# Kernel optimization log

Measured on AMD Instinct MI355X. Metric: run time of the kernel, lower is better.

The kernel has to match this reference:

```python
import jax, jax.numpy as jnp
import numpy as np

N_NODES = 100000
N_EDGES = 640000
NODE_DIM = 128
EDGE_DIM = 64
NUM_HEADS = 4
EPS = 1e-6


def setup_inputs() -> dict:
    key = jax.random.key(0)
    ks = jax.random.split(key, 12)
    s_attn = 1.0 / np.sqrt(NODE_DIM + EDGE_DIM)
    s_ev = 1.0 / np.sqrt(EDGE_DIM)
    s_out = 1.0 / np.sqrt(NODE_DIM)
    return {
        "node_features": jax.random.normal(ks[0], (N_NODES, NODE_DIM), jnp.float32),
        "edge_features": jax.random.normal(ks[1], (N_EDGES, EDGE_DIM), jnp.float32),
        "attn_W": jax.random.uniform(ks[2], (NODE_DIM + EDGE_DIM, NUM_HEADS), jnp.float32, -s_attn, s_attn),
        "attn_b": jax.random.uniform(ks[3], (NUM_HEADS,), jnp.float32, -s_attn, s_attn),
        "ev_W": jax.random.uniform(ks[4], (EDGE_DIM, NODE_DIM), jnp.float32, -s_ev, s_ev),
        "ev_b": jax.random.uniform(ks[5], (NODE_DIM,), jnp.float32, -s_ev, s_ev),
        "out1_W": jax.random.uniform(ks[6], (NODE_DIM, NODE_DIM), jnp.float32, -s_out, s_out),
        "out1_b": jax.random.uniform(ks[7], (NODE_DIM,), jnp.float32, -s_out, s_out),
        "out2_W": jax.random.uniform(ks[8], (NODE_DIM, NODE_DIM), jnp.float32, -s_out, s_out),
        "out2_b": jax.random.uniform(ks[9], (NODE_DIM,), jnp.float32, -s_out, s_out),
        "edge_index": jax.random.randint(ks[10], (2, N_EDGES), 0, N_NODES, jnp.int64 if jax.config.jax_enable_x64 else jnp.int32),
    }


def _segment_softmax_aggregate(values, scores_mean, dst, num_nodes):
    # segment max (empty segments -> -inf, then zeroed, matching torch include_self=False path)
    max_scores = jax.ops.segment_max(scores_mean, dst, num_segments=num_nodes)
    max_scores = jnp.where(jnp.isneginf(max_scores), jnp.zeros_like(max_scores), max_scores)
    exp_scores = jnp.exp(scores_mean - max_scores[dst])            # (E,)
    sum_exp = jax.ops.segment_sum(exp_scores, dst, num_segments=num_nodes)
    attn_weights = exp_scores / (sum_exp[dst] + EPS)               # (E,)
    # weighted scatter-add of edge values into destination nodes
    return jax.ops.segment_sum(values * attn_weights[:, None], dst, num_segments=num_nodes)


def reference(node_features, edge_features, attn_W, attn_b, ev_W, ev_b,
              out1_W, out1_b, out2_W, out2_b, edge_index):
    num_nodes = node_features.shape[0]
    dst = edge_index[1]
    h_dst = node_features[dst]                                     # (E, node_dim) gather
    attn_input = jnp.concatenate([h_dst, edge_features], axis=1)   # (E, node_dim+edge_dim)
    attn_scores = attn_input @ attn_W + attn_b                     # (E, H)
    scores_mean = attn_scores.mean(axis=1)                         # (E,)
    edge_values = edge_features @ ev_W + ev_b                      # (E, node_dim)
    messages = _segment_softmax_aggregate(edge_values, scores_mean, dst, num_nodes)
    update = jax.nn.relu(messages @ out1_W + out1_b) @ out2_W + out2_b
    return node_features + update
```

## Files before the change

kernel.cpp:

```cpp
#include <hip/hip_runtime.h>
#include <cstddef>

#define NN 100000
#define NE 640000
#define NB_SCAN 391
#define NTILE 1563

typedef short  short8   __attribute__((ext_vector_type(8)));
typedef float  f32x4    __attribute__((ext_vector_type(4)));
typedef ushort ushort4v __attribute__((ext_vector_type(4)));

__device__ __forceinline__ short f2bf(float f) {
    union { float f; unsigned u; } v; v.f = f;
    unsigned r = (v.u + 0x7fffu + ((v.u >> 16) & 1u)) >> 16;
    return (short)r;
}

__global__ __launch_bounds__(256) void k_init(
    int4* __restrict__ zp, const float* __restrict__ evW,
    const float* __restrict__ evb, const float* __restrict__ W1,
    ushort* __restrict__ EVW1t, float* __restrict__ EVB1)
{
    const int b = blockIdx.x;
    if (b < 196) {
        const int i = b * 256 + threadIdx.x;
        if (i < 50000) zp[i] = make_int4(0, 0, 0, 0);
        return;
    }
    if (threadIdx.x >= 128) return;
    const int j = b - 196;
    const int n = threadIdx.x;
    float acc = 0.f;
    #pragma unroll 8
    for (int c = 0; c < 128; ++c)
        acc = fmaf(evW[j * 128 + c], W1[c * 128 + n], acc);
    EVW1t[n * 64 + j] = (ushort)f2bf(acc);
    if (j == 0) {
        float ab = 0.f;
        #pragma unroll 8
        for (int c = 0; c < 128; ++c)
            ab = fmaf(evb[c], W1[c * 128 + n], ab);
        EVB1[n] = ab;
    }
}

__global__ __launch_bounds__(256) void k_pre(
    const float* __restrict__ W2, const int* __restrict__ dst_idx,
    int* __restrict__ count, ushort* __restrict__ W2t)
{
    const int gid = blockIdx.x * 256 + threadIdx.x;
    if (gid < 16384) {
        const int n = gid >> 7, k = gid & 127;
        W2t[gid] = (ushort)f2bf(W2[k * 128 + n]);
    }
    atomicAdd(&count[dst_idx[gid]], 1);
}

__global__ __launch_bounds__(256) void k_scan_bsum(
    const int* __restrict__ count, int* __restrict__ bsum)
{
    __shared__ int s[256];
    const int t = threadIdx.x, i = blockIdx.x * 256 + t;
    s[t] = (i < NN) ? count[i] : 0;
    __syncthreads();
    for (int off = 128; off; off >>= 1) { if (t < off) s[t] += s[t + off]; __syncthreads(); }
    if (t == 0) bsum[blockIdx.x] = s[0];
}

__global__ __launch_bounds__(256) void k_scan_final(
    const int* __restrict__ count, const int* __restrict__ bsum,
    int* __restrict__ rowptr)
{
    __shared__ int s[256];
    __shared__ int red[4];
    const int t = threadIdx.x, i = blockIdx.x * 256 + t;
    const int v = (i < NN) ? count[i] : 0;
    s[t] = v;

    int part = 0;
    for (int b = t; b < blockIdx.x; b += 256) part += bsum[b];
    #pragma unroll
    for (int off = 32; off; off >>= 1) part += __shfl_xor(part, off);
    if ((t & 63) == 0) red[t >> 6] = part;
    __syncthreads();
    const int boff = red[0] + red[1] + red[2] + red[3];

    for (int off = 1; off < 256; off <<= 1) {
        const int x = (t >= off) ? s[t - off] : 0;
        __syncthreads();
        s[t] += x;
        __syncthreads();
    }
    if (i < NN) rowptr[i] = boff + s[t] - v;
    if (blockIdx.x == NB_SCAN - 1 && t == 255) rowptr[NN] = boff + s[255];
}

__global__ __launch_bounds__(256) void k_permute(
    const int* __restrict__ dst_idx, const int* __restrict__ rowptr,
    int* cursor, int* __restrict__ perm)
{
    const int e = blockIdx.x * 256 + threadIdx.x;
    const int dd = dst_idx[e];
    perm[rowptr[dd] + atomicAdd(&cursor[dd], 1)] = e;
}

__global__ __launch_bounds__(256, 8) void k_agg_gather(
    const float* __restrict__ ef, const float* __restrict__ attn_W,
    const int* __restrict__ perm, const int* __restrict__ rowptr,
    ushort* __restrict__ agg, float* __restrict__ msum)
{
    const int t  = threadIdx.x;
    const int sl = t & 15;
    const int n  = blockIdx.x * 16 + (t >> 4);
    const int beg = rowptr[n], end = rowptr[n + 1];

    float4 wl;
    {
        const float4 r0 = *reinterpret_cast<const float4*>(attn_W + (128 + sl * 4 + 0) * 4);
        const float4 r1 = *reinterpret_cast<const float4*>(attn_W + (128 + sl * 4 + 1) * 4);
        const float4 r2 = *reinterpret_cast<const float4*>(attn_W + (128 + sl * 4 + 2) * 4);
        const float4 r3 = *reinterpret_cast<const float4*>(attn_W + (128 + sl * 4 + 3) * 4);
        wl.x = 0.25f * (r0.x + r0.y + r0.z + r0.w);
        wl.y = 0.25f * (r1.x + r1.y + r1.z + r1.w);
        wl.z = 0.25f * (r2.x + r2.y + r2.z + r2.w);
        wl.w = 0.25f * (r3.x + r3.y + r3.z + r3.w);
    }

    float m  = -3.0e38f;
    float se = 0.f;
    f32x4 acc = {0.f, 0.f, 0.f, 0.f};

    for (int i = beg; i < end; i += 6) {
        int pe[6];
        #pragma unroll
        for (int j = 0; j < 6; ++j)
            pe[j] = perm[(i + j < end) ? (i + j) : beg];
        float4 v[6];
        #pragma unroll
        for (int j = 0; j < 6; ++j)
            v[j] = *reinterpret_cast<const float4*>(ef + (size_t)pe[j] * 64 + sl * 4);
        float sc[6];
        #pragma unroll
        for (int j = 0; j < 6; ++j) {
            float x = v[j].x * wl.x + v[j].y * wl.y + v[j].z * wl.z + v[j].w * wl.w;
            #pragma unroll
            for (int off = 8; off; off >>= 1) x += __shfl_xor(x, off, 16);
            sc[j] = (i + j < end) ? x : -3.0e38f;
        }
        float bm = m;
        #pragma unroll
        for (int j = 0; j < 6; ++j) bm = fmaxf(bm, sc[j]);
        const float r = __expf(m - bm);
        acc[0] *= r; acc[1] *= r; acc[2] *= r; acc[3] *= r; se *= r;
        m = bm;
        #pragma unroll
        for (int j = 0; j < 6; ++j) {
            const float w = __expf(sc[j] - m);
            acc[0] = fmaf(w, v[j].x, acc[0]);
            acc[1] = fmaf(w, v[j].y, acc[1]);
            acc[2] = fmaf(w, v[j].z, acc[2]);
            acc[3] = fmaf(w, v[j].w, acc[3]);
            se += w;
        }
    }

    ushort4v o;
    o[0] = (ushort)f2bf(acc[0]); o[1] = (ushort)f2bf(acc[1]);
    o[2] = (ushort)f2bf(acc[2]); o[3] = (ushort)f2bf(acc[3]);
    *reinterpret_cast<ushort4v*>(agg + (size_t)n * 64 + sl * 4) = o;
    if (sl == 0) msum[n] = se;
}

__global__ __launch_bounds__(256, 2) void k_mega(
    const ushort* __restrict__ agg, const float* __restrict__ msum,
    const ushort* __restrict__ EVW1t, const float* __restrict__ EVB1,
    const float* __restrict__ b1, const ushort* __restrict__ W2t,
    const float* __restrict__ b2, const float* __restrict__ nf,
    float* __restrict__ out)
{
    __shared__ ushort wev[128 * 64];
    __shared__ ushort ww2[128 * 128];
    __shared__ ushort tl[4][16][136];

    const int tid  = threadIdx.x;
    const int wid  = tid >> 6;
    const int lane = tid & 63;
    const int r    = lane & 15;
    const int g    = lane >> 4;

    for (int c = tid; c < 1024; c += 256) {
        const int n = c >> 3, k8 = c & 7;
        *reinterpret_cast<short8*>(&wev[n * 64 + ((k8 ^ (n & 7)) * 8)]) =
            *reinterpret_cast<const short8*>(EVW1t + n * 64 + k8 * 8);
    }
    for (int c = tid; c < 2048; c += 256) {
        const int n = c >> 4, k8 = c & 15;
        *reinterpret_cast<short8*>(&ww2[n * 128 + ((k8 ^ (n & 7)) * 8)]) =
            *reinterpret_cast<const short8*>(W2t + n * 128 + k8 * 8);
    }
    __syncthreads();

    float evb1c[8], b1c[8], b2c[8];
    #pragma unroll
    for (int nt = 0; nt < 8; ++nt) {
        evb1c[nt] = EVB1[nt * 16 + r];
        b1c[nt]   = b1[nt * 16 + r];
        b2c[nt]   = b2[nt * 16 + r];
    }

    for (int bt = blockIdx.x; bt < NTILE; bt += gridDim.x) {
        const int n0 = bt * 64 + wid * 16;
        if (n0 >= NN) continue;

        const short8 aev0 = *reinterpret_cast<const short8*>(agg + (size_t)(n0 + r) * 64 + g * 8);
        const short8 aev1 = *reinterpret_cast<const short8*>(agg + (size_t)(n0 + r) * 64 + 32 + g * 8);
        float cf[4], cb[4];
        #pragma unroll
        for (int i = 0; i < 4; ++i) {
            const float s = msum[n0 + g * 4 + i];
            const float c = 1.f / (s + 1e-6f);
            cf[i] = c; cb[i] = s * c;
        }

        #pragma unroll
        for (int nt = 0; nt < 8; ++nt) {
            const int row = nt * 16 + r;
            const short8 w0 = *reinterpret_cast<const short8*>(
                &wev[row * 64 + (((0 + g) ^ (r & 7)) * 8)]);
            const short8 w1 = *reinterpret_cast<const short8*>(
                &wev[row * 64 + (((4 + g) ^ (r & 7)) * 8)]);
            f32x4 acc = {0.f, 0.f, 0.f, 0.f};
            acc = __builtin_amdgcn_mfma_f32_16x16x32_bf16(aev0, w0, acc, 0, 0, 0);
            acc = __builtin_amdgcn_mfma_f32_16x16x32_bf16(aev1, w1, acc, 0, 0, 0);
            #pragma unroll
            for (int i = 0; i < 4; ++i) {
                const float h = fmaxf(cf[i] * acc[i] + cb[i] * evb1c[nt] + b1c[nt], 0.f);
                tl[wid][g * 4 + i][nt * 16 + r] = (ushort)f2bf(h);
            }
        }
        asm volatile("s_waitcnt lgkmcnt(0)" ::: "memory");

        short8 a2[4];
        #pragma unroll
        for (int t = 0; t < 4; ++t)
            a2[t] = *reinterpret_cast<const short8*>(&tl[wid][r][t * 32 + g * 8]);
        asm volatile("s_waitcnt lgkmcnt(0)" ::: "memory");

        #pragma unroll
        for (int nt = 0; nt < 8; ++nt) {
            f32x4 acc = {0.f, 0.f, 0.f, 0.f};
            #pragma unroll
            for (int t = 0; t < 4; ++t) {
                const short8 w = *reinterpret_cast<const short8*>(
                    &ww2[(nt * 16 + r) * 128 + (((t * 4 + g) ^ (r & 7)) * 8)]);
                acc = __builtin_amdgcn_mfma_f32_16x16x32_bf16(a2[t], w, acc, 0, 0, 0);
            }
            #pragma unroll
            for (int i = 0; i < 4; ++i) {
                const size_t idx = (size_t)(n0 + g * 4 + i) * 128 + nt * 16 + r;
                out[idx] = nf[idx] + acc[i] + b2c[nt];
            }
        }
    }
}

extern "C" void kernel_launch(void* const* d_in, const int* in_sizes, int n_in,
                              void* d_out, int out_size, void* d_ws, size_t ws_size,
                              hipStream_t stream)
{
    const float* nf     = (const float*)d_in[0];
    const float* ef     = (const float*)d_in[1];
    const float* attn_W = (const float*)d_in[2];
    const float* evW    = (const float*)d_in[4];
    const float* evb    = (const float*)d_in[5];
    const float* W1     = (const float*)d_in[6];
    const float* b1     = (const float*)d_in[7];
    const float* W2     = (const float*)d_in[8];
    const float* b2     = (const float*)d_in[9];
    const int*   eidx   = (const int*)d_in[10];
    const int*   dst    = eidx + NE;
    float* out = (float*)d_out;

    char* ws = (char*)d_ws;
    int*    count  = (int*)   (ws + 0);
    int*    cursor = (int*)   (ws + 400000);
    int*    rowptr = (int*)   (ws + 800000);
    float*  msum   = (float*) (ws + 1200128);
    int*    perm   = (int*)   (ws + 1600128);
    ushort* agg    = (ushort*)(ws + 4160128);
    ushort* W2t    = (ushort*)(ws + 16960128);
    ushort* EVW1t  = (ushort*)(ws + 16992896);
    float*  EVB1   = (float*) (ws + 17009280);
    int*    bsum   = (int*)   (ws + 17009792);

    k_init       <<<260,  256, 0, stream>>>((int4*)count, evW, evb, W1, EVW1t, EVB1);
    k_pre        <<<2500, 256, 0, stream>>>(W2, dst, count, W2t);
    k_scan_bsum  <<<NB_SCAN, 256, 0, stream>>>(count, bsum);
    k_scan_final <<<NB_SCAN, 256, 0, stream>>>(count, bsum, rowptr);
    k_permute    <<<2500, 256, 0, stream>>>(dst, rowptr, cursor, perm);
    k_agg_gather <<<6250, 256, 0, stream>>>(ef, attn_W, perm, rowptr, agg, msum);
    k_mega       <<<521,  256, 0, stream>>>(agg, msum, EVW1t, EVB1, b1, W2t, b2, nf, out);
}
```

Baseline: 144.8 us.

## Software-pipeline k_mega tiles with register prefetch of agg, msum and node features

The grid-stride loop in the final MLP kernel becomes three fixed, unrolled tile stages. The next tile's aggregated messages, softmax sums and residual node features are loaded into registers while the current tile's MFMA work runs, and the first tile's loads are issued before the weights are staged into LDS. This is meant to hide global-memory latency, including the residual nf read that previously sat on the store path. It costs many more live registers (two tiles' worth, including 32 floats of nf each) under launch_bounds(256,2), which risks spilling, and it hardcodes three tiles per block to match the grid of 521.

```diff
diff --git a/kernel.cpp b/kernel.cpp
--- a/kernel.cpp
+++ b/kernel.cpp
@@ -5,6 +5,7 @@
 #define NE 640000
 #define NB_SCAN 391
 #define NTILE 1563
+#define MGRID 521
 
 typedef short  short8   __attribute__((ext_vector_type(8)));
 typedef float  f32x4    __attribute__((ext_vector_type(4)));
@@ -171,6 +172,85 @@
     if (sl == 0) msum[n] = se;
 }
 
+struct TileRegs {
+    short8 a0, a1;
+    float cf0, cf1, cf2, cf3;
+    float cb0, cb1, cb2, cb3;
+    float nfv[32];
+};
+
+__device__ __forceinline__ void tl_load(
+    TileRegs& T, const ushort* __restrict__ agg, const float* __restrict__ msum,
+    const float* __restrict__ nf, int n0, int r, int g)
+{
+    T.a0 = *reinterpret_cast<const short8*>(agg + (size_t)(n0 + r) * 64 + g * 8);
+    T.a1 = *reinterpret_cast<const short8*>(agg + (size_t)(n0 + r) * 64 + 32 + g * 8);
+    const float s0 = msum[n0 + g * 4 + 0];
+    const float s1 = msum[n0 + g * 4 + 1];
+    const float s2 = msum[n0 + g * 4 + 2];
+    const float s3 = msum[n0 + g * 4 + 3];
+    T.cf0 = 1.f / (s0 + 1e-6f); T.cb0 = s0 * T.cf0;
+    T.cf1 = 1.f / (s1 + 1e-6f); T.cb1 = s1 * T.cf1;
+    T.cf2 = 1.f / (s2 + 1e-6f); T.cb2 = s2 * T.cf2;
+    T.cf3 = 1.f / (s3 + 1e-6f); T.cb3 = s3 * T.cf3;
+    #pragma unroll
+    for (int nt = 0; nt < 8; ++nt)
+        #pragma unroll
+        for (int i = 0; i < 4; ++i)
+            T.nfv[nt * 4 + i] = nf[(size_t)(n0 + g * 4 + i) * 128 + nt * 16 + r];
+}
+
+__device__ __forceinline__ void tl_compute(
+    const TileRegs& T, const ushort* __restrict__ wev,
+    const ushort* __restrict__ ww2, ushort* __restrict__ tlw,
+    const float* __restrict__ evb1c, const float* __restrict__ b1c,
+    const float* __restrict__ b2c, float* __restrict__ out,
+    int n0, int r, int g)
+{
+    const float cf[4] = {T.cf0, T.cf1, T.cf2, T.cf3};
+    const float cb[4] = {T.cb0, T.cb1, T.cb2, T.cb3};
+
+    #pragma unroll
+    for (int nt = 0; nt < 8; ++nt) {
+        const int row = nt * 16 + r;
+        const short8 w0 = *reinterpret_cast<const short8*>(
+            &wev[row * 64 + (((0 + g) ^ (r & 7)) * 8)]);
+        const short8 w1 = *reinterpret_cast<const short8*>(
+            &wev[row * 64 + (((4 + g) ^ (r & 7)) * 8)]);
+        f32x4 acc = {0.f, 0.f, 0.f, 0.f};
+        acc = __builtin_amdgcn_mfma_f32_16x16x32_bf16(T.a0, w0, acc, 0, 0, 0);
+        acc = __builtin_amdgcn_mfma_f32_16x16x32_bf16(T.a1, w1, acc, 0, 0, 0);
+        #pragma unroll
+        for (int i = 0; i < 4; ++i) {
+            const float h = fmaxf(cf[i] * acc[i] + cb[i] * evb1c[nt] + b1c[nt], 0.f);
+            tlw[(g * 4 + i) * 136 + nt * 16 + r] = (ushort)f2bf(h);
+        }
+    }
+    asm volatile("s_waitcnt lgkmcnt(0)" ::: "memory");
+
+    short8 a2[4];
+    #pragma unroll
+    for (int t = 0; t < 4; ++t)
+        a2[t] = *reinterpret_cast<const short8*>(&tlw[r * 136 + t * 32 + g * 8]);
+    asm volatile("s_waitcnt lgkmcnt(0)" ::: "memory");
+
+    #pragma unroll
+    for (int nt = 0; nt < 8; ++nt) {
+        f32x4 acc = {0.f, 0.f, 0.f, 0.f};
+        #pragma unroll
+        for (int t = 0; t < 4; ++t) {
+            const short8 w = *reinterpret_cast<const short8*>(
+                &ww2[(nt * 16 + r) * 128 + (((t * 4 + g) ^ (r & 7)) * 8)]);
+            acc = __builtin_amdgcn_mfma_f32_16x16x32_bf16(a2[t], w, acc, 0, 0, 0);
+        }
+        #pragma unroll
+        for (int i = 0; i < 4; ++i) {
+            const size_t idx = (size_t)(n0 + g * 4 + i) * 128 + nt * 16 + r;
+            out[idx] = T.nfv[nt * 4 + i] + acc[i] + b2c[nt];
+        }
+    }
+}
+
 __global__ __launch_bounds__(256, 2) void k_mega(
     const ushort* __restrict__ agg, const float* __restrict__ msum,
     const ushort* __restrict__ EVW1t, const float* __restrict__ EVB1,
@@ -188,6 +268,17 @@
     const int r    = lane & 15;
     const int g    = lane >> 4;
 
+    const int bt0 = blockIdx.x;
+    const int bt1 = bt0 + MGRID;
+    const int bt2 = bt0 + 2 * MGRID;
+    const int n00 = bt0 * 64 + wid * 16;
+    const int n01 = bt1 * 64 + wid * 16;
+    const int n02 = bt2 * 64 + wid * 16;
+    const bool a0 = n00 < NN, a1 = n01 < NN, a2v = n02 < NN;
+
+    TileRegs tA, tB, tC;
+    if (a0) tl_load(tA, agg, msum, nf, n00, r, g);
+
     for (int c = tid; c < 1024; c += 256) {
         const int n = c >> 3, k8 = c & 7;
         *reinterpret_cast<short8*>(&wev[n * 64 + ((k8 ^ (n & 7)) * 8)]) =
@@ -208,60 +299,13 @@
         b2c[nt]   = b2[nt * 16 + r];
     }
 
-    for (int bt = blockIdx.x; bt < NTILE; bt += gridDim.x) {
-        const int n0 = bt * 64 + wid * 16;
-        if (n0 >= NN) continue;
-
-        const short8 aev0 = *reinterpret_cast<const short8*>(agg + (size_t)(n0 + r) * 64 + g * 8);
-        const short8 aev1 = *reinterpret_cast<const short8*>(agg + (size_t)(n0 + r) * 64 + 32 + g * 8);
-        float cf[4], cb[4];
-        #pragma unroll
-        for (int i = 0; i < 4; ++i) {
-            const float s = msum[n0 + g * 4 + i];
-            const float c = 1.f / (s + 1e-6f);
-            cf[i] = c; cb[i] = s * c;
-        }
-
-        #pragma unroll
-        for (int nt = 0; nt < 8; ++nt) {
-            const int row = nt * 16 + r;
-            const short8 w0 = *reinterpret_cast<const short8*>(
-                &wev[row * 64 + (((0 + g) ^ (r & 7)) * 8)]);
-            const short8 w1 = *reinterpret_cast<const short8*>(
-                &wev[row * 64 + (((4 + g) ^ (r & 7)) * 8)]);
-            f32x4 acc = {0.f, 0.f, 0.f, 0.f};
-            acc = __builtin_amdgcn_mfma_f32_16x16x32_bf16(aev0, w0, acc, 0, 0, 0);
-            acc = __builtin_amdgcn_mfma_f32_16x16x32_bf16(aev1, w1, acc, 0, 0, 0);
-            #pragma unroll
-            for (int i = 0; i < 4; ++i) {
-                const float h = fmaxf(cf[i] * acc[i] + cb[i] * evb1c[nt] + b1c[nt], 0.f);
-                tl[wid][g * 4 + i][nt * 16 + r] = (ushort)f2bf(h);
-            }
-        }
-        asm volatile("s_waitcnt lgkmcnt(0)" ::: "memory");
-
-        short8 a2[4];
-        #pragma unroll
-        for (int t = 0; t < 4; ++t)
-            a2[t] = *reinterpret_cast<const short8*>(&tl[wid][r][t * 32 + g * 8]);
-        asm volatile("s_waitcnt lgkmcnt(0)" ::: "memory");
-
-        #pragma unroll
-        for (int nt = 0; nt < 8; ++nt) {
-            f32x4 acc = {0.f, 0.f, 0.f, 0.f};
-            #pragma unroll
-            for (int t = 0; t < 4; ++t) {
-                const short8 w = *reinterpret_cast<const short8*>(
-                    &ww2[(nt * 16 + r) * 128 + (((t * 4 + g) ^ (r & 7)) * 8)]);
-                acc = __builtin_amdgcn_mfma_f32_16x16x32_bf16(a2[t], w, acc, 0, 0, 0);
-            }
-            #pragma unroll
-            for (int i = 0; i < 4; ++i) {
-                const size_t idx = (size_t)(n0 + g * 4 + i) * 128 + nt * 16 + r;
-                out[idx] = nf[idx] + acc[i] + b2c[nt];
-            }
-        }
-    }
+    ushort* tlw = &tl[wid][0][0];
+
+    if (a1) tl_load(tB, agg, msum, nf, n01, r, g);
+    if (a0) tl_compute(tA, wev, ww2, tlw, evb1c, b1c, b2c, out, n00, r, g);
+    if (a2v) tl_load(tC, agg, msum, nf, n02, r, g);
+    if (a1) tl_compute(tB, wev, ww2, tlw, evb1c, b1c, b2c, out, n01, r, g);
+    if (a2v) tl_compute(tC, wev, ww2, tlw, evb1c, b1c, b2c, out, n02, r, g);
 }
 
 extern "C" void kernel_launch(void* const* d_in, const int* in_sizes, int n_in,
@@ -299,5 +343,5 @@
     k_scan_final <<<NB_SCAN, 256, 0, stream>>>(count, bsum, rowptr);
     k_permute    <<<2500, 256, 0, stream>>>(dst, rowptr, cursor, perm);
     k_agg_gather <<<6250, 256, 0, stream>>>(ef, attn_W, perm, rowptr, agg, msum);
-    k_mega       <<<521,  256, 0, stream>>>(agg, msum, EVW1t, EVB1, b1, W2t, b2, nf, out);
-}
+    k_mega       <<<MGRID, 256, 0, stream>>>(agg, msum, EVW1t, EVB1, b1, W2t, b2, nf, out);
+}
```

Result: no change. 142.9 us (-1.3%).
